# Kernel optimization log

Measured on AMD Instinct MI355X. Metric: run time of the kernel, lower is better.

The kernel has to match this reference:

```python
import jax, jax.numpy as jnp
import numpy as np

N_NODES = 100000
N_EDGES = 1250000
IN_DIM = 64
HID_DIM = 64
OUT_DIM = 64
NEG_SLOPE = 0.2
EPS = 1e-16  # PyG softmax denominator epsilon


def _xavier(key, shape):
    fan_in, fan_out = shape[1], shape[0]
    lim = jnp.sqrt(6.0 / (fan_in + fan_out))
    return jax.random.uniform(key, shape, jnp.float32, -lim, lim)


def setup_inputs() -> dict:
    key = jax.random.key(0)
    ks = jax.random.split(key, 10)
    x = jax.random.normal(ks[0], (N_NODES, IN_DIM), jnp.float32)
    edge_index = jax.random.randint(ks[1], (2, N_EDGES), 0, N_NODES, jnp.int64)
    edge_attr = jax.random.uniform(ks[2], (N_EDGES,), jnp.float32)
    # layer 1 params (torch Linear weight layout: [out, in])
    W1 = _xavier(ks[3], (HID_DIM, IN_DIM))
    a_src1 = _xavier(ks[4], (1, HID_DIM))[0]
    a_dst1 = _xavier(ks[5], (1, HID_DIM))[0]
    # layer 2 params
    W2 = _xavier(ks[6], (OUT_DIM, HID_DIM))
    a_src2 = _xavier(ks[7], (1, OUT_DIM))[0]
    a_dst2 = _xavier(ks[8], (1, OUT_DIM))[0]
    return {"x": x, "edge_index": edge_index, "edge_attr": edge_attr,
            "W1": W1, "a_src1": a_src1, "a_dst1": a_dst1,
            "W2": W2, "a_src2": a_src2, "a_dst2": a_dst2}


def gat_layer(x, W, a_src, a_dst, src, dst, edge_weight, num_nodes):
    # linear (no bias): h = x @ W^T, h: [N, out]
    h = x @ W.T
    s_src = h @ a_src  # [N]
    s_dst = h @ a_dst  # [N]
    # per-edge raw score; note j = edge_index[0] (src), i = edge_index[1] (dst)
    alpha = s_src[src] + s_dst[dst]  # [E]
    alpha = jnp.where(alpha >= 0, alpha, NEG_SLOPE * alpha)  # leaky_relu
    # segment softmax over destination nodes
    seg_max = jax.ops.segment_max(alpha, dst, num_segments=num_nodes)
    alpha = jnp.exp(alpha - seg_max[dst])
    seg_sum = jax.ops.segment_sum(alpha, dst, num_segments=num_nodes)
    alpha = alpha / (seg_sum[dst] + EPS)
    alpha = alpha * edge_weight
    # weighted scatter-add aggregation of source features
    msg = h[src] * alpha[:, None]  # [E, out]
    return jax.ops.segment_sum(msg, dst, num_segments=num_nodes)


def reference(x, edge_index, edge_attr, W1, a_src1, a_dst1, W2, a_src2, a_dst2):
    src = edge_index[0]
    dst = edge_index[1]
    h = gat_layer(x, W1, a_src1, a_dst1, src, dst, edge_attr, N_NODES)
    h = jax.nn.relu(h)
    out = gat_layer(h, W2, a_src2, a_dst2, src, dst, edge_attr, N_NODES)
    return out
```

## Files before the change

kernel.cpp:

```cpp
#include <hip/hip_runtime.h>

#define NN 100000
#define NE 1250000
#define DIM 64

#define BSHIFT 8
#define BNODES (1 << BSHIFT)
#define NBUCK ((NN + BNODES - 1) / BNODES)
#define BIN_BLOCKS 256
#define BIN_CHUNK ((NE + BIN_BLOCKS - 1) / BIN_BLOCKS)
#define BCAP 4096

typedef unsigned short bf16_t;
typedef __attribute__((ext_vector_type(8))) short short8;
typedef __attribute__((ext_vector_type(8))) unsigned short ushort8;
typedef __attribute__((ext_vector_type(4))) float f32x4;

static __device__ __forceinline__ bf16_t f2bf(float f) {
    union { float f; unsigned int u; } c; c.f = f;
    unsigned int u = c.u;
    u += 0x7FFFu + ((u >> 16) & 1u);
    return (bf16_t)(u >> 16);
}
static __device__ __forceinline__ float bf2f(bf16_t b) {
    union { unsigned int u; float f; } c; c.u = ((unsigned int)b) << 16;
    return c.f;
}

union ABFrag { short8 v; short s[8]; };

template<bool IN_BF16, bool RELU_IN>
static __device__ __forceinline__
void linear_body(int bid, const void* __restrict__ xin,
                 const float* __restrict__ W,
                 const float* __restrict__ a_src,
                 const float* __restrict__ a_dst,
                 bf16_t* __restrict__ h,
                 float* __restrict__ s_src,
                 float* __restrict__ s_dst)
{
    int tid  = threadIdx.x;
    int lane = tid & 63;
    int wid  = tid >> 6;
    int lr   = lane & 15;
    int lg   = lane >> 4;
    int rowbase = bid * 128 + wid * 16;

    ABFrag Bf[4][2];
#pragma unroll
    for (int t = 0; t < 4; ++t)
#pragma unroll
    for (int s = 0; s < 2; ++s) {
        const f32x4* wp = reinterpret_cast<const f32x4*>(W + (lr + 16*t)*DIM + 32*s + 8*lg);
        f32x4 w0 = wp[0], w1 = wp[1];
#pragma unroll
        for (int j = 0; j < 4; ++j) {
            Bf[t][s].s[j]     = (short)f2bf(w0[j]);
            Bf[t][s].s[j + 4] = (short)f2bf(w1[j]);
        }
    }

    int arow = rowbase + lr;
    if (arow > NN - 1) arow = NN - 1;

    ABFrag Af[2];
    if (IN_BF16) {
        const bf16_t* xp = (const bf16_t*)xin + (size_t)arow * DIM + 8*lg;
#pragma unroll
        for (int s = 0; s < 2; ++s) {
            ushort8 xv = *reinterpret_cast<const ushort8*>(xp + 32*s);
#pragma unroll
            for (int j = 0; j < 8; ++j) {
                unsigned short b = xv[j];
                if (RELU_IN) b = (b & 0x8000u) ? (unsigned short)0 : b;
                Af[s].s[j] = (short)b;
            }
        }
    } else {
        const float* xp = (const float*)xin + (size_t)arow * DIM + 8*lg;
#pragma unroll
        for (int s = 0; s < 2; ++s) {
            const f32x4* xq = reinterpret_cast<const f32x4*>(xp + 32*s);
            f32x4 x0 = xq[0], x1 = xq[1];
#pragma unroll
            for (int j = 0; j < 4; ++j) {
                float f0 = x0[j], f1 = x1[j];
                if (RELU_IN) { f0 = f0 > 0.f ? f0 : 0.f; f1 = f1 > 0.f ? f1 : 0.f; }
                Af[s].s[j]     = (short)f2bf(f0);
                Af[s].s[j + 4] = (short)f2bf(f1);
            }
        }
    }

    f32x4 acc[4] = {{0.f,0.f,0.f,0.f},{0.f,0.f,0.f,0.f},{0.f,0.f,0.f,0.f},{0.f,0.f,0.f,0.f}};
#pragma unroll
    for (int s = 0; s < 2; ++s)
#pragma unroll
    for (int t = 0; t < 4; ++t)
        acc[t] = __builtin_amdgcn_mfma_f32_16x16x32_bf16(Af[s].v, Bf[t][s].v, acc[t], 0, 0, 0);

    float av[4], dv[4];
#pragma unroll
    for (int t = 0; t < 4; ++t) { av[t] = a_src[lr + 16*t]; dv[t] = a_dst[lr + 16*t]; }

    float ssv[4], sdv[4];
#pragma unroll
    for (int r = 0; r < 4; ++r) {
        int row = rowbase + 4*lg + r;
        bool ok = row < NN;
        float ps = 0.f, pd = 0.f;
#pragma unroll
        for (int t = 0; t < 4; ++t) {
            float v = acc[t][r];
            ps += v * av[t];
            pd += v * dv[t];
            if (ok) h[(size_t)row * DIM + lr + 16*t] = f2bf(v);
        }
#pragma unroll
        for (int off = 8; off; off >>= 1) {
            ps += __shfl_xor(ps, off, 64);
            pd += __shfl_xor(pd, off, 64);
        }
        ssv[r] = ps; sdv[r] = pd;
    }
    if (lr == 0) {
#pragma unroll
        for (int r = 0; r < 4; ++r) {
            int row = rowbase + 4*lg + r;
            if (row < NN) { s_src[row] = ssv[r]; s_dst[row] = sdv[r]; }
        }
    }
}

__global__ __launch_bounds__(512)
void bin_hist(const int* __restrict__ dst, int* __restrict__ gcnt)
{
    __shared__ int cnt[NBUCK];
    int tid = threadIdx.x;
    for (int i = tid; i < NBUCK; i += 512) cnt[i] = 0;
    __syncthreads();
    int lo = blockIdx.x * BIN_CHUNK;
    int hi = lo + BIN_CHUNK; if (hi > NE) hi = NE;
    for (int e = lo + tid; e < hi; e += 512)
        atomicAdd(&cnt[dst[e] >> BSHIFT], 1);
    __syncthreads();
    for (int i = tid; i < NBUCK; i += 512)
        gcnt[i * BIN_BLOCKS + blockIdx.x] = cnt[i];
}

__global__ __launch_bounds__(256)
void row_scan(int* __restrict__ gcnt, int* __restrict__ btot)
{
    __shared__ int wpart[4];
    int b    = blockIdx.x;
    int tid  = threadIdx.x;
    int lane = tid & 63;
    int v = gcnt[b * BIN_BLOCKS + tid];
    int sc = v;
#pragma unroll
    for (int off = 1; off <= 32; off <<= 1) {
        int t = __shfl_up(sc, off, 64);
        if (lane >= off) sc += t;
    }
    if (lane == 63) wpart[tid >> 6] = sc;
    __syncthreads();
    if (tid == 0) {
        int run = 0;
#pragma unroll
        for (int k = 0; k < 4; ++k) { int t = wpart[k]; wpart[k] = run; run += t; }
    }
    __syncthreads();
    int incl = sc + wpart[tid >> 6];
    gcnt[b * BIN_BLOCKS + tid] = incl - v;
    if (tid == BIN_BLOCKS - 1) btot[b] = incl;
}

__global__ __launch_bounds__(512)
void scatter_linear1(const int* __restrict__ src, const int* __restrict__ dst,
                     const float* __restrict__ ea,
                     const int* __restrict__ gcnt, const int* __restrict__ btot,
                     int2* __restrict__ region,
                     const float* __restrict__ x, const float* __restrict__ W1,
                     const float* __restrict__ as1, const float* __restrict__ ad1,
                     bf16_t* __restrict__ h,
                     float* __restrict__ ssrc, float* __restrict__ sdst)
{
    if (blockIdx.x < BIN_BLOCKS) {
        __shared__ int2 sbuf[BIN_CHUNK];
        __shared__ unsigned short sbkt[BIN_CHUNK];
        __shared__ int lcur[NBUCK];
        __shared__ int gout[NBUCK];
        __shared__ int wpart[8];
        int tid  = threadIdx.x;
        int lane = tid & 63;
        int blk  = blockIdx.x;

        int cntb = 0, gex = 0;
        if (tid < NBUCK) {
            gex = gcnt[tid * BIN_BLOCKS + blk];
            int nxt = (blk + 1 < BIN_BLOCKS) ? gcnt[tid * BIN_BLOCKS + blk + 1] : btot[tid];
            cntb = nxt - gex;
        }
        int sc = cntb;
#pragma unroll
        for (int off = 1; off <= 32; off <<= 1) {
            int t = __shfl_up(sc, off, 64);
            if (lane >= off) sc += t;
        }
        if (lane == 63) wpart[tid >> 6] = sc;
        __syncthreads();
        if (tid == 0) {
            int run = 0;
#pragma unroll
            for (int k = 0; k < 8; ++k) { int t = wpart[k]; wpart[k] = run; run += t; }
        }
        __syncthreads();
        int excl = sc - cntb + wpart[tid >> 6];
        if (tid < NBUCK) {
            lcur[tid] = excl;
            gout[tid] = tid * BCAP + gex - excl;
        }
        __syncthreads();

        int lo = blk * BIN_CHUNK;
        int hi = lo + BIN_CHUNK; if (hi > NE) hi = NE;
        for (int e = lo + tid; e < hi; e += 512) {
            int d = dst[e];
            int b = d >> BSHIFT;
            int pos = atomicAdd(&lcur[b], 1);
            sbuf[pos] = make_int2(src[e] | ((d & (BNODES - 1)) << 17),
                                  __float_as_int(ea[e]));
            sbkt[pos] = (unsigned short)b;
        }
        __syncthreads();

        int T = hi - lo;
        for (int i = tid; i < T; i += 512) {
            int b = sbkt[i];
            region[gout[b] + i] = sbuf[i];
        }
    } else {
        linear_body<false, false>(blockIdx.x - BIN_BLOCKS, x, W1, as1, ad1, h, ssrc, sdst);
    }
}

__global__ __launch_bounds__(512)
void linear2(const void* __restrict__ xin, const float* __restrict__ W,
             const float* __restrict__ a_src, const float* __restrict__ a_dst,
             bf16_t* __restrict__ h, float* __restrict__ s_src, float* __restrict__ s_dst)
{
    linear_body<true, true>(blockIdx.x, xin, W, a_src, a_dst, h, s_src, s_dst);
}

__global__ __launch_bounds__(256)
void build_csr(const int* __restrict__ btot,
               const int2* __restrict__ region,
               int* __restrict__ rowptr, int* __restrict__ rend,
               int2* __restrict__ csr)
{
    int b    = blockIdx.x;
    int tid  = threadIdx.x;
    int lane = tid & 63;
    int cnt  = btot[b];
    const int2* rec = region + (size_t)b * BCAP;

    __shared__ int ncnt[BNODES];
    __shared__ int curs[BNODES];
    __shared__ int wpart[4];
    ncnt[tid] = 0;
    __syncthreads();
    for (int i = tid; i < cnt; i += 256)
        atomicAdd(&ncnt[(rec[i].x >> 17) & (BNODES - 1)], 1);
    __syncthreads();

    int v = ncnt[tid];
    int sc = v;
#pragma unroll
    for (int off = 1; off <= 32; off <<= 1) {
        int t = __shfl_up(sc, off, 64);
        if (lane >= off) sc += t;
    }
    if (lane == 63) wpart[tid >> 6] = sc;
    __syncthreads();
    if (tid == 0) {
        int run = 0;
#pragma unroll
        for (int k = 0; k < 4; ++k) { int t = wpart[k]; wpart[k] = run; run += t; }
    }
    __syncthreads();
    int excl = sc - v + wpart[tid >> 6];
    int base = b * BCAP;

    int node = (b << BSHIFT) + tid;
    if (node < NN) { rowptr[node] = base + excl; rend[node] = base + excl + v; }
    curs[tid] = base + excl;
    __syncthreads();

    for (int i = tid; i < cnt; i += 256) {
        int2 r = rec[i];
        int dl = (r.x >> 17) & (BNODES - 1);
        int pos = atomicAdd(&curs[dl], 1);
        csr[pos] = make_int2(r.x & 0x1FFFF, r.y);
    }
}

template<bool OUT_BF16>
__global__ __launch_bounds__(256)
void fused_agg(const int* __restrict__ rowptr, const int* __restrict__ rend,
               const int2* __restrict__ csr,
               const float* __restrict__ ssrc, const float* __restrict__ sdst,
               const bf16_t* __restrict__ h,
               void* __restrict__ outp)
{
    int tid  = threadIdx.x;
    int lane = tid & 63;
    int wv   = tid >> 6;
    int grp  = lane >> 4;
    int lr   = lane & 15;
    int d    = blockIdx.x * 16 + wv * 4 + grp;
    bool dok = d < NN;

    int rb = 0, deg = 0;
    if (dok) { rb = rowptr[d]; deg = rend[d] - rb; }
    float sdd = dok ? sdst[d] : 0.f;

    int wmax = deg;
    wmax = max(wmax, __shfl_xor(wmax, 16, 64));
    wmax = max(wmax, __shfl_xor(wmax, 32, 64));

    float psum = 0.f;
    float ax = 0.f, ay = 0.f, az = 0.f, aw = 0.f;

#define GSWZ(J)                                                                 \
    int   sj##J = __builtin_amdgcn_ds_swizzle(s, (((J) << 5) | 0x10));          \
    float wj##J = __int_as_float(__builtin_amdgcn_ds_swizzle(wbits, (((J) << 5) | 0x10)));
#define GLOAD(J)                                                                \
    ushort4 hv##J = *reinterpret_cast<const ushort4*>(h + (size_t)sj##J * DIM + 4*lr);
#define GACC(J)                                                                 \
    ax += wj##J * bf2f(hv##J.x); ay += wj##J * bf2f(hv##J.y);                   \
    az += wj##J * bf2f(hv##J.z); aw += wj##J * bf2f(hv##J.w);

    for (int cb = 0; cb < wmax; cb += 16) {
        int idx = cb + lr;
        bool v = idx < deg;
        int2 rec = v ? csr[rb + idx] : make_int2(0, 0);
        int   s  = rec.x;
        float a  = ssrc[s] + sdd;
        a = (a >= 0.f) ? a : 0.2f * a;
        a = fminf(a, 60.f);
        float p = v ? __expf(a) : 0.f;
        float w = p * __int_as_float(rec.y);
        int wbits = __float_as_int(w);

        GSWZ(0)  GSWZ(1)  GSWZ(2)  GSWZ(3)  GSWZ(4)  GSWZ(5)  GSWZ(6)  GSWZ(7)
        GSWZ(8)  GSWZ(9)  GSWZ(10) GSWZ(11) GSWZ(12) GSWZ(13) GSWZ(14) GSWZ(15)
        GLOAD(0)  GLOAD(1)  GLOAD(2)  GLOAD(3)  GLOAD(4)  GLOAD(5)  GLOAD(6)  GLOAD(7)
        GLOAD(8)  GLOAD(9)  GLOAD(10) GLOAD(11) GLOAD(12) GLOAD(13) GLOAD(14) GLOAD(15)

        float ps = p;
#pragma unroll
        for (int off = 1; off <= 8; off <<= 1) ps += __shfl_xor(ps, off, 64);
        psum += ps;

        GACC(0)  GACC(1)  GACC(2)  GACC(3)  GACC(4)  GACC(5)  GACC(6)  GACC(7)
        GACC(8)  GACC(9)  GACC(10) GACC(11) GACC(12) GACC(13) GACC(14) GACC(15)
    }
#undef GSWZ
#undef GLOAD
#undef GACC

    if (dok) {
        float inv = 1.f / (psum + 1e-16f);
        if (OUT_BF16) {
            ushort4 o;
            o.x = f2bf(ax * inv); o.y = f2bf(ay * inv);
            o.z = f2bf(az * inv); o.w = f2bf(aw * inv);
            *reinterpret_cast<ushort4*>((bf16_t*)outp + (size_t)d * DIM + 4*lr) = o;
        } else {
            float4 o = make_float4(ax * inv, ay * inv, az * inv, aw * inv);
            *reinterpret_cast<float4*>((float*)outp + (size_t)d * DIM + 4*lr) = o;
        }
    }
}

extern "C" void kernel_launch(void* const* d_in, const int* in_sizes, int n_in,
                              void* d_out, int out_size, void* d_ws, size_t ws_size,
                              hipStream_t stream) {
    const float* x   = (const float*)d_in[0];
    const int*   ei  = (const int*)d_in[1];
    const float* ea  = (const float*)d_in[2];
    const float* W1  = (const float*)d_in[3];
    const float* as1 = (const float*)d_in[4];
    const float* ad1 = (const float*)d_in[5];
    const float* W2  = (const float*)d_in[6];
    const float* as2 = (const float*)d_in[7];
    const float* ad2 = (const float*)d_in[8];
    const int* src = ei;
    const int* dst = ei + NE;
    float* out = (float*)d_out;

    char* p = (char*)d_ws;
    auto carve = [&](size_t bytes) { char* r = p; p += (bytes + 255) & ~(size_t)255; return (void*)r; };
    bf16_t*  acc_bf = (bf16_t*)carve((size_t)NN * DIM * 2);
    bf16_t*  h      = (bf16_t*)carve((size_t)NN * DIM * 2);
    float*   ssrc   = (float*)carve((size_t)NN * 4);
    float*   sdst   = (float*)carve((size_t)NN * 4);
    int*     rowptr = (int*)carve((size_t)NN * 4);
    int*     rend   = (int*)carve((size_t)NN * 4);
    int2*    csr    = (int2*)carve((size_t)NBUCK * BCAP * 8);
    int2*    region = (int2*)carve((size_t)NBUCK * BCAP * 8);
    int*     gcnt   = (int*)carve((size_t)NBUCK * BIN_BLOCKS * 4);
    int*     btot   = (int*)carve((size_t)NBUCK * 4);

    const int GRID_LIN  = (NN + 127) / 128;
    const int GRID_NODE = (NN + 15) / 16;

    bin_hist<<<BIN_BLOCKS, 512, 0, stream>>>(dst, gcnt);
    row_scan<<<NBUCK, 256, 0, stream>>>(gcnt, btot);
    scatter_linear1<<<BIN_BLOCKS + GRID_LIN, 512, 0, stream>>>(
        src, dst, ea, gcnt, btot, region, x, W1, as1, ad1, h, ssrc, sdst);
    build_csr<<<NBUCK, 256, 0, stream>>>(btot, region, rowptr, rend, csr);

    fused_agg<true><<<GRID_NODE, 256, 0, stream>>>(rowptr, rend, csr, ssrc, sdst, h, acc_bf);

    linear2<<<GRID_LIN, 512, 0, stream>>>(acc_bf, W2, as2, ad2, h, ssrc, sdst);
    fused_agg<false><<<GRID_NODE, 256, 0, stream>>>(rowptr, rend, csr, ssrc, sdst, h, out);
}
```

Before: 130.0 us.

## Fuse layer-2 linear transform into layer-1 aggregation epilogue

The separate linear2 kernel is removed. The layer-1 aggregation kernel now applies relu to each block's 16 aggregated rows, stages them in shared memory as bf16, and multiplies them by W2 with MFMA. It also computes the layer-2 source and destination attention scores in the same epilogue. This drops one kernel launch and the write and reread of the intermediate activation, at the cost of two block syncs, per-block conversion of W2 to bf16, and double-buffered h/score arrays.

```diff
diff --git a/kernel.cpp b/kernel.cpp
--- a/kernel.cpp
+++ b/kernel.cpp
@@ -244,14 +244,6 @@
     }
 }
 
-__global__ __launch_bounds__(512)
-void linear2(const void* __restrict__ xin, const float* __restrict__ W,
-             const float* __restrict__ a_src, const float* __restrict__ a_dst,
-             bf16_t* __restrict__ h, float* __restrict__ s_src, float* __restrict__ s_dst)
-{
-    linear_body<true, true>(blockIdx.x, xin, W, a_src, a_dst, h, s_src, s_dst);
-}
-
 __global__ __launch_bounds__(256)
 void build_csr(const int* __restrict__ btot,
                const int2* __restrict__ region,
@@ -304,14 +296,21 @@
     }
 }
 
-template<bool OUT_BF16>
+template<bool FUSE_LIN2>
 __global__ __launch_bounds__(256)
 void fused_agg(const int* __restrict__ rowptr, const int* __restrict__ rend,
                const int2* __restrict__ csr,
                const float* __restrict__ ssrc, const float* __restrict__ sdst,
                const bf16_t* __restrict__ h,
-               void* __restrict__ outp)
-{
+               const float* __restrict__ W2, const float* __restrict__ as2,
+               const float* __restrict__ ad2,
+               bf16_t* __restrict__ h2, float* __restrict__ ssrc2,
+               float* __restrict__ sdst2,
+               float* __restrict__ outp)
+{
+    __shared__ bf16_t rowbuf[16][72];
+    __shared__ float sps[4][16], spd[4][16];
+
     int tid  = threadIdx.x;
     int lane = tid & 63;
     int wv   = tid >> 6;
@@ -369,16 +368,67 @@
 #undef GLOAD
 #undef GACC
 
-    if (dok) {
-        float inv = 1.f / (psum + 1e-16f);
-        if (OUT_BF16) {
-            ushort4 o;
-            o.x = f2bf(ax * inv); o.y = f2bf(ay * inv);
-            o.z = f2bf(az * inv); o.w = f2bf(aw * inv);
-            *reinterpret_cast<ushort4*>((bf16_t*)outp + (size_t)d * DIM + 4*lr) = o;
-        } else {
+    if (!FUSE_LIN2) {
+        if (dok) {
+            float inv = 1.f / (psum + 1e-16f);
             float4 o = make_float4(ax * inv, ay * inv, az * inv, aw * inv);
-            *reinterpret_cast<float4*>((float*)outp + (size_t)d * DIM + 4*lr) = o;
+            *reinterpret_cast<float4*>(outp + (size_t)d * DIM + 4*lr) = o;
+        }
+        return;
+    }
+
+    {
+        float inv = dok ? 1.f / (psum + 1e-16f) : 0.f;
+        float r0 = ax * inv, r1 = ay * inv, r2 = az * inv, r3 = aw * inv;
+        r0 = r0 > 0.f ? r0 : 0.f;  r1 = r1 > 0.f ? r1 : 0.f;
+        r2 = r2 > 0.f ? r2 : 0.f;  r3 = r3 > 0.f ? r3 : 0.f;
+        int ns = wv * 4 + grp;
+        ushort4 pk;
+        pk.x = f2bf(r0); pk.y = f2bf(r1); pk.z = f2bf(r2); pk.w = f2bf(r3);
+        *reinterpret_cast<ushort4*>(&rowbuf[ns][4 * lr]) = pk;
+    }
+    __syncthreads();
+
+    int lg = lane >> 4;
+    ABFrag Af2[2];
+#pragma unroll
+    for (int s = 0; s < 2; ++s)
+        Af2[s].v = *reinterpret_cast<const short8*>(&rowbuf[lr][32 * s + 8 * lg]);
+    ABFrag Bf2[2];
+#pragma unroll
+    for (int s = 0; s < 2; ++s) {
+        const f32x4* wp = reinterpret_cast<const f32x4*>(W2 + (lr + 16 * wv) * DIM + 32 * s + 8 * lg);
+        f32x4 w0 = wp[0], w1 = wp[1];
+#pragma unroll
+        for (int j = 0; j < 4; ++j) {
+            Bf2[s].s[j]     = (short)f2bf(w0[j]);
+            Bf2[s].s[j + 4] = (short)f2bf(w1[j]);
+        }
+    }
+    f32x4 a2 = {0.f, 0.f, 0.f, 0.f};
+    a2 = __builtin_amdgcn_mfma_f32_16x16x32_bf16(Af2[0].v, Bf2[0].v, a2, 0, 0, 0);
+    a2 = __builtin_amdgcn_mfma_f32_16x16x32_bf16(Af2[1].v, Bf2[1].v, a2, 0, 0, 0);
+
+    float av = as2[lr + 16 * wv], dv = ad2[lr + 16 * wv];
+#pragma unroll
+    for (int r = 0; r < 4; ++r) {
+        int ns = 4 * lg + r;
+        int node = blockIdx.x * 16 + ns;
+        if (node < NN) h2[(size_t)node * DIM + lr + 16 * wv] = f2bf(a2[r]);
+        float cs = a2[r] * av, cd = a2[r] * dv;
+#pragma unroll
+        for (int off = 8; off; off >>= 1) {
+            cs += __shfl_xor(cs, off, 64);
+            cd += __shfl_xor(cd, off, 64);
+        }
+        if (lr == 0) { sps[wv][ns] = cs; spd[wv][ns] = cd; }
+    }
+    __syncthreads();
+    if (tid < 16) {
+        int node = blockIdx.x * 16 + tid;
+        if (node < NN) {
+            ssrc2[node] = sps[0][tid] + sps[1][tid] + sps[2][tid] + sps[3][tid];
+            sdst2[node] = spd[0][tid] + spd[1][tid] + spd[2][tid] + spd[3][tid];
         }
     }
 }
@@ -401,10 +451,12 @@
 
     char* p = (char*)d_ws;
     auto carve = [&](size_t bytes) { char* r = p; p += (bytes + 255) & ~(size_t)255; return (void*)r; };
-    bf16_t*  acc_bf = (bf16_t*)carve((size_t)NN * DIM * 2);
+    bf16_t*  h2     = (bf16_t*)carve((size_t)NN * DIM * 2);
     bf16_t*  h      = (bf16_t*)carve((size_t)NN * DIM * 2);
     float*   ssrc   = (float*)carve((size_t)NN * 4);
     float*   sdst   = (float*)carve((size_t)NN * 4);
+    float*   ssrc2  = (float*)carve((size_t)NN * 4);
+    float*   sdst2  = (float*)carve((size_t)NN * 4);
     int*     rowptr = (int*)carve((size_t)NN * 4);
     int*     rend   = (int*)carve((size_t)NN * 4);
     int2*    csr    = (int2*)carve((size_t)NBUCK * BCAP * 8);
@@ -421,8 +473,10 @@
         src, dst, ea, gcnt, btot, region, x, W1, as1, ad1, h, ssrc, sdst);
     build_csr<<<NBUCK, 256, 0, stream>>>(btot, region, rowptr, rend, csr);
 
-    fused_agg<true><<<GRID_NODE, 256, 0, stream>>>(rowptr, rend, csr, ssrc, sdst, h, acc_bf);
-
-    linear2<<<GRID_LIN, 512, 0, stream>>>(acc_bf, W2, as2, ad2, h, ssrc, sdst);
-    fused_agg<false><<<GRID_NODE, 256, 0, stream>>>(rowptr, rend, csr, ssrc, sdst, h, out);
-}
+    fused_agg<true><<<GRID_NODE, 256, 0, stream>>>(
+        rowptr, rend, csr, ssrc, sdst, h, W2, as2, ad2, h2, ssrc2, sdst2, nullptr);
+
+    fused_agg<false><<<GRID_NODE, 256, 0, stream>>>(
+        rowptr, rend, csr, ssrc2, sdst2, h2, nullptr, nullptr, nullptr,
+        nullptr, nullptr, nullptr, out);
+}
```

Result: faster. 119.5 us, median of 2 (-8.0%).
